# Optimization experiments

Hardware: AMD Instinct MI355X
Metric: run time of the kernel (lower is better)

The kernel has to match this reference:

```python
import jax, jax.numpy as jnp
import numpy as np

B, H, V, L, T = 64, 512, 32000, 3, 38
SOS = 0  # word2idx['<SOS>']


def setup_inputs() -> dict:
    key = jax.random.key(0)
    ks = jax.random.split(key, 16)
    s = 0.05
    rn = lambda k, shape: jax.random.normal(k, shape, jnp.float32) * s
    return {
        "feat": jax.random.normal(ks[0], (B, H), jnp.float32),
        "W_ih0": rn(ks[1], (4 * H, 2 * H)),
        "W_hh0": rn(ks[2], (4 * H, H)),
        "W_ih_rest": rn(ks[3], (L - 1, 4 * H, H)),
        "W_hh_rest": rn(ks[4], (L - 1, 4 * H, H)),
        "b_ih": rn(ks[5], (L, 4 * H)),
        "b_hh": rn(ks[6], (L, 4 * H)),
        "embed": rn(ks[7], (V, H)),
        "W_proj": rn(ks[8], (V, H)),
        "b_proj": rn(ks[9], (V,)),
        "W_hid": rn(ks[10], (H, H)),
        "b_hid": rn(ks[11], (H,)),
        "W_enc": rn(ks[12], (H, H)),
        "b_enc": rn(ks[13], (H,)),
        "W_attout": rn(ks[14], (1, H)),
        "b_attout": rn(ks[15], (1,)),
    }


def _lstm_cell(x, h, c, Wih, Whh, bih, bhh):
    # PyTorch gate order: i, f, g, o
    g = x @ Wih.T + h @ Whh.T + bih + bhh
    i, f, gg, o = jnp.split(g, 4, axis=-1)
    c2 = jax.nn.sigmoid(f) * c + jax.nn.sigmoid(i) * jnp.tanh(gg)
    h2 = jax.nn.sigmoid(o) * jnp.tanh(c2)
    return h2, c2


def _forward(feat, W_ih0, W_hh0, W_ih_rest, W_hh_rest, b_ih, b_hh,
             embed, W_proj, b_proj, W_hid, b_hid, W_enc, b_enc,
             W_attout, b_attout):
    # encoder 'sequence': pooled feature repeated over L decoder layers -> [L,B,H]
    enc = jnp.broadcast_to(feat[None], (L, B, H))
    enc_p = enc @ W_enc.T + b_enc  # precompute encoder projection (constant over steps)

    def attn(hbar):  # hbar = sum(hidden_layers)/L, [B,H]  (Bahdanau additive attention)
        e = (jnp.tanh(enc_p + (hbar @ W_hid.T + b_hid)[None]) @ W_attout.T + b_attout)[..., 0]  # [L,B]
        w = jax.nn.softmax(e, axis=0)  # softmax over encoder positions
        return jnp.einsum('lb,lbh->bh', w, enc)  # context [B,H]

    def lstm(inp, h, c):  # one time-step through the 3-layer stacked LSTM
        h0, c0 = _lstm_cell(inp, h[0], c[0], W_ih0, W_hh0, b_ih[0], b_hh[0])
        h1, c1 = _lstm_cell(h0, h[1], c[1], W_ih_rest[0], W_hh_rest[0], b_ih[1], b_hh[1])
        h2, c2 = _lstm_cell(h1, h[2], c[2], W_ih_rest[1], W_hh_rest[1], b_ih[2], b_hh[2])
        return jnp.stack([h0, h1, h2]), jnp.stack([c0, c1, c2])

    ctx0 = attn(feat)  # initial hidden = feat repeated L times -> mean = feat
    start = jnp.broadcast_to(embed[SOS], (B, H))
    h = jnp.broadcast_to(ctx0[None], (L, B, H))
    c = h
    inp0 = jnp.concatenate([ctx0, start], axis=-1)  # [B, 2H]

    def step(carry, _):
        h, c, inp = carry
        h, c = lstm(inp, h, c)
        out = h[-1]  # [B,H]
        ids = jnp.argmax(out @ W_proj.T + b_proj, axis=-1)  # greedy token (dropout in eval mode)
        emb = embed[ids]  # [B,H]
        ctx = attn(emb / L)  # addMask averages with 1/decoder_layer weights
        return (h, c, jnp.concatenate([ctx, emb], axis=-1)), out

    _, outs = jax.lax.scan(step, (h, c, inp0), None, length=T - 1)  # outs [T-1,B,H]
    pred = jnp.concatenate([start[None], outs], axis=0)  # [T,B,H]
    # final projection, permuted to [B, V, T] as in the torch module
    return jnp.einsum('tbh,vh->bvt', pred, W_proj) + b_proj[None, :, None]


def reference(feat, W_ih0, W_hh0, W_ih_rest, W_hh_rest, b_ih, b_hh,
              embed, W_proj, b_proj, W_hid, b_hid, W_enc, b_enc,
              W_attout, b_attout):
    return _forward(feat, W_ih0, W_hh0, W_ih_rest, W_hh_rest, b_ih, b_hh,
                    embed, W_proj, b_proj, W_hid, b_hid, W_enc, b_enc,
                    W_attout, b_attout)
```

## Files before the change

kernel.cpp:

```cpp
#include <hip/hip_runtime.h>
#include <hip/hip_bf16.h>

#define B   64
#define H   512
#define V   32000
#define T   38
#define G4  2048
#define NSTEP 37
#define VT  64
#define KC  64
#define LDP 68
#define NTILE 250
#define DELTA 0.008f
#define MAXC 128

typedef __attribute__((ext_vector_type(8))) short short8;
typedef __attribute__((ext_vector_type(4))) float f32x4;
typedef unsigned long long ull;

__device__ __forceinline__ float sigf(float x){ return 1.0f/(1.0f + expf(-x)); }

__device__ __forceinline__ unsigned int fkey(float x){
  unsigned int u = __float_as_uint(x);
  return (u & 0x80000000u) ? ~u : (u | 0x80000000u);
}
__device__ __forceinline__ float fromkey(unsigned int k){
  unsigned int u = (k & 0x80000000u) ? (k & 0x7fffffffu) : ~k;
  return __uint_as_float(u);
}
__device__ __forceinline__ ull mkkey(float v, int idx){
  return ((ull)fkey(v)<<32) | (ull)(unsigned int)(~(unsigned int)idx);
}
__device__ __forceinline__ unsigned short f2bf(float x){
  unsigned int u = __float_as_uint(x);
  unsigned int r = (u + 0x7FFFu + ((u >> 16) & 1u)) >> 16;
  return (unsigned short)r;
}
__device__ __forceinline__ float bf2f(unsigned short u){
  return __uint_as_float((unsigned int)u << 16);
}

__global__ __launch_bounds__(256) void k_init_state(const float* __restrict__ feat,
                                                    float* __restrict__ hT, float* __restrict__ cT,
                                                    ull* __restrict__ packed){
  int idx = blockIdx.x*blockDim.x + threadIdx.x;
  if (idx < 3*H*B){
    int b = idx & (B-1);
    int k = (idx >> 6) & (H-1);
    float v = feat[(size_t)b*H + k];
    hT[idx] = v;
    cT[idx] = v;
  }
  if (idx < NSTEP*B) packed[idx] = 0ULL;
}

__global__ __launch_bounds__(256) void k_convW(const float* __restrict__ src,
                                               unsigned short* __restrict__ hi){
  int i = blockIdx.x*blockDim.x + threadIdx.x;
  float4 f = ((const float4*)src)[i];
  ushort4 h4 = make_ushort4(f2bf(f.x), f2bf(f.y), f2bf(f.z), f2bf(f.w));
  ((ushort4*)hi)[i] = h4;
}

__global__ __launch_bounds__(256) void k_gfeat(const float* __restrict__ feat,
                                               const float* __restrict__ Wih0,
                                               const float* __restrict__ b_ih,
                                               const float* __restrict__ b_hh,
                                               float* __restrict__ gfeatT){
  int j = blockIdx.x;
  int b = threadIdx.x;
  int gate = threadIdx.y;
  int r = gate*H + j;
  const float* w = Wih0 + (size_t)r*(2*H);
  const float* x = feat + (size_t)b*H;
  float acc = 0.f;
  #pragma unroll 4
  for (int k=0;k<H;k++) acc = fmaf(w[k], x[k], acc);
  gfeatT[((size_t)gate*H + j)*B + b] = acc + b_ih[r] + b_hh[r];
}

__global__ __launch_bounds__(256) void k_row0(const float* __restrict__ embed_,
                                              const float* __restrict__ Wp,
                                              const float* __restrict__ bp,
                                              unsigned short* __restrict__ dstBf,
                                              float* __restrict__ dstF, int mode){
  int v = blockIdx.x*blockDim.x + threadIdx.x;
  if (v >= V) return;
  const float4* e = (const float4*)embed_;
  const float4* w = (const float4*)(Wp + (size_t)v*H);
  float acc = 0.f;
  #pragma unroll 4
  for (int k=0;k<H/4;k++){
    float4 a = e[k], c = w[k];
    acc += a.x*c.x + a.y*c.y + a.z*c.z + a.w*c.w;
  }
  acc += bp[v];
  if (mode == 0){
    unsigned short bv = f2bf(acc);
    for (int b=0;b<B;b++) __builtin_nontemporal_store(bv, dstBf + (size_t)b*V + v);
  } else {
    for (int b=0;b<B;b++) dstF[((size_t)b*V + v)*T] = acc;
  }
}

__global__ __launch_bounds__(256) void k_lstm(int layer, int s,
    const float* __restrict__ Wih, const float* __restrict__ Whh,
    const float* __restrict__ bias_ih, const float* __restrict__ bias_hh,
    const float* __restrict__ gfeatT,
    const float* __restrict__ embed_,
    const ull* __restrict__ packedPrev,
    const float* __restrict__ xLowerT,
    const float* __restrict__ hOldT,
    float* __restrict__ hNewT,
    float* __restrict__ cT_,
    unsigned short* __restrict__ hBf,
    float* __restrict__ hF)
{
  const int j  = blockIdx.x;
  const int b  = threadIdx.x;
  const int ks = threadIdx.y;
  __shared__ float part[4][4][B];

  const int kbase = (ks & 1)*256;
  const float *w0,*w1,*w2,*w3;
  const float* xptr = nullptr;
  const float* eptr = nullptr;

  if (ks < 2){
    if (layer == 0){
      const size_t gs = (size_t)H*(2*H);
      w0 = Wih + (size_t)j*(2*H) + H + kbase;
      w1 = w0 + gs; w2 = w0 + 2*gs; w3 = w0 + 3*gs;
      int er = 0;
      if (s > 0) er = (int)(~(unsigned int)(packedPrev[b] & 0xFFFFFFFFull));
      eptr = embed_ + (size_t)er*H + kbase;
    } else {
      const size_t gs = (size_t)H*H;
      w0 = Wih + (size_t)j*H + kbase;
      w1 = w0 + gs; w2 = w0 + 2*gs; w3 = w0 + 3*gs;
      xptr = xLowerT + (size_t)kbase*B + b;
    }
  } else {
    const size_t gs = (size_t)H*H;
    w0 = Whh + (size_t)j*H + kbase;
    w1 = w0 + gs; w2 = w0 + 2*gs; w3 = w0 + 3*gs;
    xptr = hOldT + (size_t)kbase*B + b;
  }

  float a0=0.f, a1=0.f, a2=0.f, a3=0.f;
  if (eptr){
    #pragma unroll 4
    for (int k=0;k<256;k++){
      float xv = eptr[k];
      a0 = fmaf(w0[k], xv, a0); a1 = fmaf(w1[k], xv, a1);
      a2 = fmaf(w2[k], xv, a2); a3 = fmaf(w3[k], xv, a3);
    }
  } else {
    #pragma unroll 4
    for (int k=0;k<256;k++){
      float xv = xptr[(size_t)k*B];
      a0 = fmaf(w0[k], xv, a0); a1 = fmaf(w1[k], xv, a1);
      a2 = fmaf(w2[k], xv, a2); a3 = fmaf(w3[k], xv, a3);
    }
  }
  part[ks][0][b]=a0; part[ks][1][b]=a1; part[ks][2][b]=a2; part[ks][3][b]=a3;
  __syncthreads();

  if (ks == 0){
    float g[4];
    #pragma unroll
    for (int gt=0; gt<4; gt++){
      float sum = part[0][gt][b] + part[1][gt][b] + part[2][gt][b] + part[3][gt][b];
      if (layer == 0) sum += gfeatT[((size_t)gt*H + j)*B + b];
      else            sum += bias_ih[gt*H + j] + bias_hh[gt*H + j];
      g[gt] = sum;
    }
    float i_ = sigf(g[0]);
    float f_ = sigf(g[1]);
    float gg = tanhf(g[2]);
    float o_ = sigf(g[3]);
    float cold = cT_[(size_t)j*B + b];
    float c2 = f_*cold + i_*gg;
    float h2 = o_*tanhf(c2);
    cT_[(size_t)j*B + b]  = c2;
    hNewT[(size_t)j*B + b] = h2;
    if (hBf) hBf[(size_t)b*H + j] = f2bf(h2);
    if (hF)  hF [(size_t)b*H + j] = h2;
  }
}

__global__ __launch_bounds__(256) void k_logits_mfma(
    const unsigned short* __restrict__ Wbf,
    const unsigned short* __restrict__ h2bf,
    const float* __restrict__ bp,
    unsigned short* __restrict__ dst,
    ull* __restrict__ tilemax)
{
  const int tid  = threadIdx.x;
  const int wave = tid >> 6;
  const int lane = tid & 63;
  const int col  = lane & 15;
  const int grp  = lane >> 4;
  const int v0   = blockIdx.x*128 + wave*32;

  f32x4 acc[4][2] = {{{0.f,0.f,0.f,0.f},{0.f,0.f,0.f,0.f}},
                     {{0.f,0.f,0.f,0.f},{0.f,0.f,0.f,0.f}},
                     {{0.f,0.f,0.f,0.f},{0.f,0.f,0.f,0.f}},
                     {{0.f,0.f,0.f,0.f},{0.f,0.f,0.f,0.f}}};

  const unsigned short* hp = h2bf + (size_t)col*H + grp*8;
  const unsigned short* wp = Wbf  + (size_t)(v0+col)*H + grp*8;

  for (int k0 = 0; k0 < H; k0 += 32){
    short8 afr[4], bfr[2];
    #pragma unroll
    for (int bt=0;bt<4;bt++)
      afr[bt] = *(const short8*)(hp + (size_t)bt*16*H + k0);
    #pragma unroll
    for (int vt=0;vt<2;vt++)
      bfr[vt] = *(const short8*)(wp + (size_t)vt*16*H + k0);
    #pragma unroll
    for (int bt=0;bt<4;bt++)
      #pragma unroll
      for (int vt=0;vt<2;vt++)
        acc[bt][vt] = __builtin_amdgcn_mfma_f32_16x16x32_bf16(afr[bt], bfr[vt], acc[bt][vt], 0,0,0);
  }

  float bias0 = bp[v0 + col];
  float bias1 = bp[v0 + 16 + col];

  ull keys[4][4];
  #pragma unroll
  for (int bt=0;bt<4;bt++){
    #pragma unroll
    for (int r=0;r<4;r++){
      int b = bt*16 + grp*4 + r;
      float val0 = acc[bt][0][r] + bias0;
      float val1 = acc[bt][1][r] + bias1;
      __builtin_nontemporal_store(f2bf(val0), dst + (size_t)b*V + v0 + col);
      __builtin_nontemporal_store(f2bf(val1), dst + (size_t)b*V + v0 + 16 + col);
      float m; int mv;
      if (val1 > val0){ m = val1; mv = v0+16+col; } else { m = val0; mv = v0+col; }
      keys[bt][r] = mkkey(m, mv);
    }
  }
  #pragma unroll
  for (int bt=0;bt<4;bt++)
    #pragma unroll
    for (int r=0;r<4;r++){
      ull k2 = keys[bt][r];
      #pragma unroll
      for (int m=1;m<16;m<<=1){
        ull o = __shfl_xor(k2, m, 64);
        if (o > k2) k2 = o;
      }
      keys[bt][r] = k2;
    }

  __shared__ ull wred[4][64];
  if (col == 0){
    #pragma unroll
    for (int bt=0;bt<4;bt++)
      #pragma unroll
      for (int r=0;r<4;r++)
        wred[wave][bt*16 + grp*4 + r] = keys[bt][r];
  }
  __syncthreads();
  if (tid < 64){
    ull best = wred[0][tid];
    #pragma unroll
    for (int w=1;w<4;w++) if (wred[w][tid] > best) best = wred[w][tid];
    tilemax[(size_t)tid*NTILE + blockIdx.x] = best;
  }
}

__global__ __launch_bounds__(256) void k_rescue(
    const unsigned short* __restrict__ plane,
    const ull* __restrict__ tilemax,
    const float* __restrict__ hF,
    const float* __restrict__ Wp,
    const float* __restrict__ bp,
    ull* __restrict__ packedS)
{
  const int b    = blockIdx.x;
  const int tid  = threadIdx.x;
  const int lane = tid & 63;
  const int wave = tid >> 6;

  __shared__ float hrow[H];
  __shared__ ull   keybuf[256];
  __shared__ int   tlist[NTILE];
  __shared__ int   vlist[MAXC];
  __shared__ ull   ckey[MAXC];
  __shared__ int   tcount, vcount;

  for (int k=tid; k<H; k+=256) hrow[k] = hF[(size_t)b*H + k];
  ull myk = (tid < NTILE) ? tilemax[(size_t)b*NTILE + tid] : 0ULL;
  keybuf[tid] = myk;
  if (tid == 0){ tcount = 0; vcount = 0; }
  __syncthreads();
  #pragma unroll
  for (int st=128; st>0; st>>=1){
    if (tid < st){ ull o = keybuf[tid+st]; if (o > keybuf[tid]) keybuf[tid] = o; }
    __syncthreads();
  }
  const float gmax   = fromkey((unsigned int)(keybuf[0] >> 32));
  const float thresh = gmax - DELTA;

  if (tid < NTILE && fromkey((unsigned int)(myk >> 32)) >= thresh){
    int i = atomicAdd(&tcount, 1); tlist[i] = tid;
  }
  __syncthreads();

  const int nt = tcount;
  for (int ti=0; ti<nt; ti++){
    if (tid < 128){
      int v = tlist[ti]*128 + tid;
      float val = bf2f(plane[(size_t)b*V + v]);
      if (val >= thresh){
        int i = atomicAdd(&vcount, 1);
        if (i < MAXC) vlist[i] = v;
      }
    }
  }
  __syncthreads();
  const int nc = min(vcount, MAXC);

  for (int base=0; base<nc; base+=4){
    int i = base + wave;
    if (i < nc){
      int v = vlist[i];
      const float* wrow = Wp + (size_t)v*H;
      float acc = 0.f;
      #pragma unroll
      for (int k=lane; k<H; k+=64) acc = fmaf(wrow[k], hrow[k], acc);
      #pragma unroll
      for (int m=32; m>0; m>>=1) acc += __shfl_xor(acc, m, 64);
      if (lane == 0) ckey[i] = mkkey(acc + bp[v], v);
    }
  }
  __syncthreads();
  if (tid == 0){
    ull best = 0ULL;
    for (int i=0;i<nc;i++) if (ckey[i] > best) best = ckey[i];
    packedS[b] = best;
  }
}

__global__ __launch_bounds__(256) void k_logits(
    const float* __restrict__ h2T,
    const float* __restrict__ Wp,
    const float* __restrict__ bp,
    float* __restrict__ dst, int strideV, int strideB,
    ull* __restrict__ packedS)
{
  __shared__ float Wt[KC][LDP];
  __shared__ float Xt[KC][LDP];
  __shared__ ull red[B][17];

  const int tid = threadIdx.x;
  const int v0  = blockIdx.x * VT;
  const int tv  = tid & 15;
  const int tb  = tid >> 4;
  const int vr  = tid >> 2;
  const int kq  = tid & 3;

  float acc[4][4];
  #pragma unroll
  for (int i=0;i<4;i++)
    #pragma unroll
    for (int q=0;q<4;q++) acc[i][q] = 0.f;

  for (int k0=0; k0<H; k0+=KC){
    __syncthreads();
    const float* wsrc = Wp + (size_t)(v0+vr)*H + k0 + kq*16;
    #pragma unroll
    for (int i=0;i<4;i++){
      float4 w4 = *(const float4*)(wsrc + i*4);
      int kk = kq*16 + i*4;
      Wt[kk+0][vr]=w4.x; Wt[kk+1][vr]=w4.y; Wt[kk+2][vr]=w4.z; Wt[kk+3][vr]=w4.w;
    }
    const float* xsrc = h2T + (size_t)(k0+vr)*B + kq*16;
    #pragma unroll
    for (int i=0;i<4;i++){
      float4 x4 = *(const float4*)(xsrc + i*4);
      int bb = kq*16 + i*4;
      Xt[vr][bb+0]=x4.x; Xt[vr][bb+1]=x4.y; Xt[vr][bb+2]=x4.z; Xt[vr][bb+3]=x4.w;
    }
    __syncthreads();
    #pragma unroll 8
    for (int k=0;k<KC;k++){
      float4 w4 = *(const float4*)&Wt[k][tv<<2];
      float4 x4 = *(const float4*)&Xt[k][tb<<2];
      acc[0][0]=fmaf(x4.x,w4.x,acc[0][0]); acc[0][1]=fmaf(x4.x,w4.y,acc[0][1]);
      acc[0][2]=fmaf(x4.x,w4.z,acc[0][2]); acc[0][3]=fmaf(x4.x,w4.w,acc[0][3]);
      acc[1][0]=fmaf(x4.y,w4.x,acc[1][0]); acc[1][1]=fmaf(x4.y,w4.y,acc[1][1]);
      acc[1][2]=fmaf(x4.y,w4.z,acc[1][2]); acc[1][3]=fmaf(x4.y,w4.w,acc[1][3]);
      acc[2][0]=fmaf(x4.z,w4.x,acc[2][0]); acc[2][1]=fmaf(x4.z,w4.y,acc[2][1]);
      acc[2][2]=fmaf(x4.z,w4.z,acc[2][2]); acc[2][3]=fmaf(x4.z,w4.w,acc[2][3]);
      acc[3][0]=fmaf(x4.w,w4.x,acc[3][0]); acc[3][1]=fmaf(x4.w,w4.y,acc[3][1]);
      acc[3][2]=fmaf(x4.w,w4.z,acc[3][2]); acc[3][3]=fmaf(x4.w,w4.w,acc[3][3]);
    }
  }

  float4 bb4 = *(const float4*)(bp + v0 + (tv<<2));
  float barr[4] = {bb4.x, bb4.y, bb4.z, bb4.w};
  float vals[4][4];
  #pragma unroll
  for (int bj=0;bj<4;bj++)
    #pragma unroll
    for (int vi=0;vi<4;vi++) vals[bj][vi] = acc[bj][vi] + barr[vi];

  #pragma unroll
  for (int bj=0;bj<4;bj++){
    int b = (tb<<2)+bj;
    #pragma unroll
    for (int vi=0;vi<4;vi++)
      dst[(size_t)b*strideB + (size_t)(v0+(tv<<2)+vi)*strideV] = vals[bj][vi];
  }

  #pragma unroll
  for (int bj=0;bj<4;bj++){
    float m = vals[bj][0]; int mi = v0+(tv<<2);
    #pragma unroll
    for (int vi=1;vi<4;vi++){
      if (vals[bj][vi] > m){ m = vals[bj][vi]; mi = v0+(tv<<2)+vi; }
    }
    red[(tb<<2)+bj][tv] = mkkey(m, mi);
  }
  __syncthreads();
  if (tid < B){
    ull best = red[tid][0];
    #pragma unroll
    for (int t2=1;t2<16;t2++){ ull k2 = red[tid][t2]; if (k2 > best) best = k2; }
    atomicMax(packedS + tid, best);
  }
}

__global__ __launch_bounds__(256) void k_transpose(const unsigned short* __restrict__ stage,
                                                   float* __restrict__ out){
  __shared__ float tile[64][40];
  const int b  = blockIdx.x / (V/64);
  const int vt = blockIdx.x % (V/64);
  const int v0 = vt*64;
  const int tid = threadIdx.x;

  for (int idx = tid; idx < T*64; idx += 256){
    int t  = idx >> 6;
    int vl = idx & 63;
    unsigned short u = __builtin_nontemporal_load(stage + (size_t)t*B*V + (size_t)b*V + v0 + vl);
    tile[vl][t] = bf2f(u);
  }
  __syncthreads();

  float* obase = out + ((size_t)b*V + v0)*T;
  for (int idx = tid; idx < (T*64)/4; idx += 256){
    int e = idx*4;
    f32x4 o;
    o[0] = tile[(e+0)/T][(e+0)%T];
    o[1] = tile[(e+1)/T][(e+1)%T];
    o[2] = tile[(e+2)/T][(e+2)%T];
    o[3] = tile[(e+3)/T][(e+3)%T];
    __builtin_nontemporal_store(o, (f32x4*)(obase + e));
  }
}

extern "C" void kernel_launch(void* const* d_in, const int* in_sizes, int n_in,
                              void* d_out, int out_size, void* d_ws, size_t ws_size,
                              hipStream_t stream){
  const float* feat      = (const float*)d_in[0];
  const float* W_ih0     = (const float*)d_in[1];
  const float* W_hh0     = (const float*)d_in[2];
  const float* W_ih_rest = (const float*)d_in[3];
  const float* W_hh_rest = (const float*)d_in[4];
  const float* b_ih      = (const float*)d_in[5];
  const float* b_hh      = (const float*)d_in[6];
  const float* embed     = (const float*)d_in[7];
  const float* W_proj    = (const float*)d_in[8];
  const float* b_proj    = (const float*)d_in[9];
  float* out = (float*)d_out;

  char* ws = (char*)d_ws;
  size_t off = 0;
  float* hT = (float*)(ws + off); off += (size_t)2*3*H*B*4;
  float* cT = (float*)(ws + off); off += (size_t)3*H*B*4;
  float* gfeatT = (float*)(ws + off); off += (size_t)4*H*B*4;
  ull* packed = (ull*)(ws + off); off += (size_t)NSTEP*B*8;
  unsigned short* h2bf = (unsigned short*)(ws + off); off += (size_t)B*H*2;
  float* hF32 = (float*)(ws + off); off += (size_t)B*H*4;
  ull* tilemax = (ull*)(ws + off); off += (size_t)B*NTILE*8;
  off = (off + 255) & ~(size_t)255;
  unsigned short* Whi = (unsigned short*)(ws + off); off += (size_t)V*H*2;
  off = (off + 255) & ~(size_t)255;
  unsigned short* stage = (unsigned short*)(ws + off);
  const size_t need = off + (size_t)T*B*V*2;
  const bool fast = (ws_size >= need);

  dim3 bl64x4(64,4);
  k_init_state<<<(3*H*B + 255)/256, 256, 0, stream>>>(feat, hT, cT, packed);
  k_gfeat<<<H, bl64x4, 0, stream>>>(feat, W_ih0, b_ih, b_hh, gfeatT);
  if (fast){
    k_convW<<<(V*H/4)/256, 256, 0, stream>>>(W_proj, Whi);
    k_row0<<<(V+255)/256, 256, 0, stream>>>(embed, W_proj, b_proj, stage, (float*)nullptr, 0);
  } else {
    k_row0<<<(V+255)/256, 256, 0, stream>>>(embed, W_proj, b_proj, (unsigned short*)nullptr, out, 1);
  }

  const size_t LHB = (size_t)H*B;
  for (int s=0; s<NSTEP; s++){
    const int p = s & 1, q = p ^ 1;
    float* hOld = hT + (size_t)p*3*LHB;
    float* hNew = hT + (size_t)q*3*LHB;
    const ull* pk = packed + (size_t)(s>0 ? s-1 : 0)*B;

    k_lstm<<<H, bl64x4, 0, stream>>>(0, s, W_ih0, W_hh0,
        b_ih, b_hh, gfeatT, embed, pk,
        (const float*)nullptr, hOld + 0*LHB, hNew + 0*LHB, cT + 0*LHB,
        (unsigned short*)nullptr, (float*)nullptr);
    k_lstm<<<H, bl64x4, 0, stream>>>(1, s, W_ih_rest, W_hh_rest,
        b_ih + 1*G4, b_hh + 1*G4, (const float*)nullptr, (const float*)nullptr,
        (const ull*)nullptr,
        hNew + 0*LHB, hOld + 1*LHB, hNew + 1*LHB, cT + 1*LHB,
        (unsigned short*)nullptr, (float*)nullptr);
    k_lstm<<<H, bl64x4, 0, stream>>>(2, s, W_ih_rest + (size_t)G4*H, W_hh_rest + (size_t)G4*H,
        b_ih + 2*G4, b_hh + 2*G4, (const float*)nullptr, (const float*)nullptr,
        (const ull*)nullptr,
        hNew + 1*LHB, hOld + 2*LHB, hNew + 2*LHB, cT + 2*LHB,
        fast ? h2bf : (unsigned short*)nullptr,
        fast ? hF32 : (float*)nullptr);

    if (fast){
      unsigned short* plane = stage + (size_t)(s+1)*B*V;
      k_logits_mfma<<<NTILE, 256, 0, stream>>>(Whi, h2bf, b_proj, plane, tilemax);
      k_rescue<<<B, 256, 0, stream>>>(plane, tilemax, hF32, W_proj, b_proj,
                                      packed + (size_t)s*B);
    } else {
      k_logits<<<V/VT, 256, 0, stream>>>(hNew + 2*LHB, W_proj, b_proj,
          out + (s+1), T, V*T, packed + (size_t)s*B);
    }
  }

  if (fast) k_transpose<<<B*(V/64), 256, 0, stream>>>(stage, out);
}
```

Before: 3.893 ms.

## Fuse argmax rescue into logits kernel via last-blocks ticket counter

Removes the separate per-step rescue launch. The logits MFMA kernel now takes an atomic ticket after writing its tile maxima. The last 16 blocks spin until all 250 tiles are done, then each handles the rescue for 4 batch rows. This trades one kernel launch per step for a spin-wait in 16 blocks and less parallelism in the rescue (16 blocks instead of 64). Correctness relies on all 250 blocks being co-resident, or at least on the last-ticket blocks not starving earlier ones.

```diff
diff --git a/kernel.cpp b/kernel.cpp
--- a/kernel.cpp
+++ b/kernel.cpp
@@ -13,6 +13,8 @@
 #define NTILE 250
 #define DELTA 0.008f
 #define MAXC 128
+#define NRG 16
+#define BPG 4
 
 typedef __attribute__((ext_vector_type(8))) short short8;
 typedef __attribute__((ext_vector_type(4))) float f32x4;
@@ -42,7 +44,8 @@
 
 __global__ __launch_bounds__(256) void k_init_state(const float* __restrict__ feat,
                                                     float* __restrict__ hT, float* __restrict__ cT,
-                                                    ull* __restrict__ packed){
+                                                    ull* __restrict__ packed,
+                                                    int* __restrict__ cnt){
   int idx = blockIdx.x*blockDim.x + threadIdx.x;
   if (idx < 3*H*B){
     int b = idx & (B-1);
@@ -52,6 +55,7 @@
     cT[idx] = v;
   }
   if (idx < NSTEP*B) packed[idx] = 0ULL;
+  if (idx < NSTEP) cnt[idx] = 0;
 }
 
 __global__ __launch_bounds__(256) void k_convW(const float* __restrict__ src,
@@ -194,7 +198,11 @@
     const unsigned short* __restrict__ h2bf,
     const float* __restrict__ bp,
     unsigned short* __restrict__ dst,
-    ull* __restrict__ tilemax)
+    ull* __restrict__ tilemax,
+    int* __restrict__ cnt,
+    const float* __restrict__ hF,
+    const float* __restrict__ WpF,
+    ull* __restrict__ packedS)
 {
   const int tid  = threadIdx.x;
   const int wave = tid >> 6;
@@ -272,78 +280,89 @@
     for (int w=1;w<4;w++) if (wred[w][tid] > best) best = wred[w][tid];
     tilemax[(size_t)tid*NTILE + blockIdx.x] = best;
   }
-}
-
-__global__ __launch_bounds__(256) void k_rescue(
-    const unsigned short* __restrict__ plane,
-    const ull* __restrict__ tilemax,
-    const float* __restrict__ hF,
-    const float* __restrict__ Wp,
-    const float* __restrict__ bp,
-    ull* __restrict__ packedS)
-{
-  const int b    = blockIdx.x;
-  const int tid  = threadIdx.x;
-  const int lane = tid & 63;
-  const int wave = tid >> 6;
+
+  asm volatile("s_waitcnt vmcnt(0)" ::: "memory");
+  __syncthreads();
+  __shared__ int ticket_s;
+  if (tid == 0)
+    ticket_s = __hip_atomic_fetch_add(cnt, 1, __ATOMIC_RELEASE, __HIP_MEMORY_SCOPE_AGENT);
+  __syncthreads();
+  const int ticket = ticket_s;
+  if (ticket < NTILE - NRG) return;
+  const int rg = ticket - (NTILE - NRG);
+
+  if (tid == 0){
+    while (__hip_atomic_load(cnt, __ATOMIC_RELAXED, __HIP_MEMORY_SCOPE_AGENT) < NTILE)
+      __builtin_amdgcn_s_sleep(2);
+  }
+  __syncthreads();
 
   __shared__ float hrow[H];
   __shared__ ull   keybuf[256];
-  __shared__ int   tlist[NTILE];
+  __shared__ int   tlist[64];
   __shared__ int   vlist[MAXC];
   __shared__ ull   ckey[MAXC];
   __shared__ int   tcount, vcount;
 
-  for (int k=tid; k<H; k+=256) hrow[k] = hF[(size_t)b*H + k];
-  ull myk = (tid < NTILE) ? tilemax[(size_t)b*NTILE + tid] : 0ULL;
-  keybuf[tid] = myk;
-  if (tid == 0){ tcount = 0; vcount = 0; }
-  __syncthreads();
-  #pragma unroll
-  for (int st=128; st>0; st>>=1){
-    if (tid < st){ ull o = keybuf[tid+st]; if (o > keybuf[tid]) keybuf[tid] = o; }
-    __syncthreads();
-  }
-  const float gmax   = fromkey((unsigned int)(keybuf[0] >> 32));
-  const float thresh = gmax - DELTA;
-
-  if (tid < NTILE && fromkey((unsigned int)(myk >> 32)) >= thresh){
-    int i = atomicAdd(&tcount, 1); tlist[i] = tid;
-  }
-  __syncthreads();
-
-  const int nt = tcount;
-  for (int ti=0; ti<nt; ti++){
-    if (tid < 128){
-      int v = tlist[ti]*128 + tid;
-      float val = bf2f(plane[(size_t)b*V + v]);
-      if (val >= thresh){
-        int i = atomicAdd(&vcount, 1);
-        if (i < MAXC) vlist[i] = v;
+  for (int bi = 0; bi < BPG; ++bi){
+    const int b = rg*BPG + bi;
+    for (int k=tid; k<H; k+=256) hrow[k] = hF[(size_t)b*H + k];
+    ull myk = 0ULL;
+    if (tid < NTILE)
+      myk = __hip_atomic_load(tilemax + (size_t)b*NTILE + tid,
+                              __ATOMIC_RELAXED, __HIP_MEMORY_SCOPE_AGENT);
+    keybuf[tid] = myk;
+    if (tid == 0){ tcount = 0; vcount = 0; }
+    __syncthreads();
+    #pragma unroll
+    for (int st=128; st>0; st>>=1){
+      if (tid < st){ ull o = keybuf[tid+st]; if (o > keybuf[tid]) keybuf[tid] = o; }
+      __syncthreads();
+    }
+    const float gmax   = fromkey((unsigned int)(keybuf[0] >> 32));
+    const float thresh = gmax - DELTA;
+
+    if (tid < NTILE && fromkey((unsigned int)(myk >> 32)) >= thresh){
+      int i = atomicAdd(&tcount, 1); if (i < 64) tlist[i] = tid;
+    }
+    __syncthreads();
+
+    const int nt = min(tcount, 64);
+    for (int ti=0; ti<nt; ++ti){
+      if (tid < 64){
+        const unsigned int* p32 = (const unsigned int*)(dst + (size_t)b*V + tlist[ti]*128);
+        unsigned int u = __hip_atomic_load((unsigned int*)(p32 + tid),
+                                           __ATOMIC_RELAXED, __HIP_MEMORY_SCOPE_AGENT);
+        int vbase = tlist[ti]*128 + 2*tid;
+        float va = bf2f((unsigned short)(u & 0xFFFFu));
+        float vb = bf2f((unsigned short)(u >> 16));
+        if (va >= thresh){ int i = atomicAdd(&vcount,1); if (i<MAXC) vlist[i] = vbase; }
+        if (vb >= thresh){ int i = atomicAdd(&vcount,1); if (i<MAXC) vlist[i] = vbase+1; }
       }
     }
-  }
-  __syncthreads();
-  const int nc = min(vcount, MAXC);
-
-  for (int base=0; base<nc; base+=4){
-    int i = base + wave;
-    if (i < nc){
-      int v = vlist[i];
-      const float* wrow = Wp + (size_t)v*H;
-      float acc = 0.f;
-      #pragma unroll
-      for (int k=lane; k<H; k+=64) acc = fmaf(wrow[k], hrow[k], acc);
-      #pragma unroll
-      for (int m=32; m>0; m>>=1) acc += __shfl_xor(acc, m, 64);
-      if (lane == 0) ckey[i] = mkkey(acc + bp[v], v);
-    }
-  }
-  __syncthreads();
-  if (tid == 0){
-    ull best = 0ULL;
-    for (int i=0;i<nc;i++) if (ckey[i] > best) best = ckey[i];
-    packedS[b] = best;
+    __syncthreads();
+    const int nc = min(vcount, MAXC);
+
+    for (int base=0; base<nc; base+=4){
+      int i = base + wave;
+      if (i < nc){
+        int v = vlist[i];
+        const float* wrow = WpF + (size_t)v*H;
+        float a = 0.f;
+        #pragma unroll
+        for (int k=lane; k<H; k+=64) a = fmaf(wrow[k], hrow[k], a);
+        #pragma unroll
+        for (int m=32; m>0; m>>=1) a += __shfl_xor(a, m, 64);
+        if (lane == 0) ckey[i] = mkkey(a + bp[v], v);
+      }
+    }
+    __syncthreads();
+    if (tid == 0){
+      ull best = 0ULL;
+      for (int i=0;i<nc;i++) if (ckey[i] > best) best = ckey[i];
+      packedS[b] = best;
+    }
+    __syncthreads();
   }
 }
 
@@ -489,6 +508,7 @@
   unsigned short* h2bf = (unsigned short*)(ws + off); off += (size_t)B*H*2;
   float* hF32 = (float*)(ws + off); off += (size_t)B*H*4;
   ull* tilemax = (ull*)(ws + off); off += (size_t)B*NTILE*8;
+  int* cnt = (int*)(ws + off); off += (size_t)NSTEP*4;
   off = (off + 255) & ~(size_t)255;
   unsigned short* Whi = (unsigned short*)(ws + off); off += (size_t)V*H*2;
   off = (off + 255) & ~(size_t)255;
@@ -497,7 +517,7 @@
   const bool fast = (ws_size >= need);
 
   dim3 bl64x4(64,4);
-  k_init_state<<<(3*H*B + 255)/256, 256, 0, stream>>>(feat, hT, cT, packed);
+  k_init_state<<<(3*H*B + 255)/256, 256, 0, stream>>>(feat, hT, cT, packed, cnt);
   k_gfeat<<<H, bl64x4, 0, stream>>>(feat, W_ih0, b_ih, b_hh, gfeatT);
   if (fast){
     k_convW<<<(V*H/4)/256, 256, 0, stream>>>(W_proj, Whi);
@@ -531,9 +551,9 @@
 
     if (fast){
       unsigned short* plane = stage + (size_t)(s+1)*B*V;
-      k_logits_mfma<<<NTILE, 256, 0, stream>>>(Whi, h2bf, b_proj, plane, tilemax);
-      k_rescue<<<B, 256, 0, stream>>>(plane, tilemax, hF32, W_proj, b_proj,
-                                      packed + (size_t)s*B);
+      k_logits_mfma<<<NTILE, 256, 0, stream>>>(Whi, h2bf, b_proj, plane, tilemax,
+                                               cnt + s, hF32, W_proj,
+                                               packed + (size_t)s*B);
     } else {
       k_logits<<<V/VT, 256, 0, stream>>>(hNew + 2*LHB, W_proj, b_proj,
           out + (s+1), T, V*T, packed + (size_t)s*B);
```

After: 4.535 ms. 1.16x slower.

## Fuse fp32 argmax rescue into MFMA logits kernel with per-tile thresholds

Applied to the files above, without the earlier changes.

Merges the separate rescue kernel into the bf16 MFMA logits kernel. Each tile now picks candidates using its own per-row tile maximum minus DELTA, recomputes their exact fp32 dot products, and combines results with atomicMax into the packed argmax. This drops one launch per decode step and the tilemax round trip through global memory. In exchange every tile rescores at least one candidate per batch row, which adds far more fp32 dot products per step. It also relies on the packed buffer being zeroed beforehand for atomicMax to work.

```diff
diff --git a/kernel.cpp b/kernel.cpp
--- a/kernel.cpp
+++ b/kernel.cpp
@@ -12,7 +12,7 @@
 #define LDP 68
 #define NTILE 250
 #define DELTA 0.008f
-#define MAXC 128
+#define VCAP 512
 
 typedef __attribute__((ext_vector_type(8))) short short8;
 typedef __attribute__((ext_vector_type(4))) float f32x4;
@@ -194,7 +194,9 @@
     const unsigned short* __restrict__ h2bf,
     const float* __restrict__ bp,
     unsigned short* __restrict__ dst,
-    ull* __restrict__ tilemax)
+    const float* __restrict__ hF,
+    const float* __restrict__ WpF,
+    ull* __restrict__ packedS)
 {
   const int tid  = threadIdx.x;
   const int wave = tid >> 6;
@@ -258,6 +260,10 @@
     }
 
   __shared__ ull wred[4][64];
+  __shared__ float bthr[B];
+  __shared__ int  vlist[VCAP];
+  __shared__ int  vcount;
+  if (tid == 0) vcount = 0;
   if (col == 0){
     #pragma unroll
     for (int bt=0;bt<4;bt++)
@@ -270,80 +276,51 @@
     ull best = wred[0][tid];
     #pragma unroll
     for (int w=1;w<4;w++) if (wred[w][tid] > best) best = wred[w][tid];
-    tilemax[(size_t)tid*NTILE + blockIdx.x] = best;
-  }
-}
-
-__global__ __launch_bounds__(256) void k_rescue(
-    const unsigned short* __restrict__ plane,
-    const ull* __restrict__ tilemax,
-    const float* __restrict__ hF,
-    const float* __restrict__ Wp,
-    const float* __restrict__ bp,
-    ull* __restrict__ packedS)
-{
-  const int b    = blockIdx.x;
-  const int tid  = threadIdx.x;
-  const int lane = tid & 63;
-  const int wave = tid >> 6;
-
-  __shared__ float hrow[H];
-  __shared__ ull   keybuf[256];
-  __shared__ int   tlist[NTILE];
-  __shared__ int   vlist[MAXC];
-  __shared__ ull   ckey[MAXC];
-  __shared__ int   tcount, vcount;
-
-  for (int k=tid; k<H; k+=256) hrow[k] = hF[(size_t)b*H + k];
-  ull myk = (tid < NTILE) ? tilemax[(size_t)b*NTILE + tid] : 0ULL;
-  keybuf[tid] = myk;
-  if (tid == 0){ tcount = 0; vcount = 0; }
+    bthr[tid] = fromkey((unsigned int)(best >> 32)) - DELTA;
+  }
   __syncthreads();
-  #pragma unroll
-  for (int st=128; st>0; st>>=1){
-    if (tid < st){ ull o = keybuf[tid+st]; if (o > keybuf[tid]) keybuf[tid] = o; }
-    __syncthreads();
-  }
-  const float gmax   = fromkey((unsigned int)(keybuf[0] >> 32));
-  const float thresh = gmax - DELTA;
-
-  if (tid < NTILE && fromkey((unsigned int)(myk >> 32)) >= thresh){
-    int i = atomicAdd(&tcount, 1); tlist[i] = tid;
+
+  #pragma unroll
+  for (int bt=0;bt<4;bt++){
+    #pragma unroll
+    for (int r=0;r<4;r++){
+      int b = bt*16 + grp*4 + r;
+      float thr = bthr[b];
+      float val0 = acc[bt][0][r] + bias0;
+      float val1 = acc[bt][1][r] + bias1;
+      #pragma unroll
+      for (int vt=0; vt<2; vt++){
+        float val = vt ? val1 : val0;
+        int v = v0 + vt*16 + col;
+        if (val >= thr){
+          int i = atomicAdd(&vcount, 1);
+          if (i < VCAP) vlist[i] = (b << 15) | v;
+          else {
+            const float* wrow = WpF + (size_t)v*H;
+            const float* hrow = hF  + (size_t)b*H;
+            float a = 0.f;
+            for (int k=0;k<H;k++) a = fmaf(wrow[k], hrow[k], a);
+            atomicMax(packedS + b, mkkey(a + bp[v], v));
+          }
+        }
+      }
+    }
   }
   __syncthreads();
-
-  const int nt = tcount;
-  for (int ti=0; ti<nt; ti++){
-    if (tid < 128){
-      int v = tlist[ti]*128 + tid;
-      float val = bf2f(plane[(size_t)b*V + v]);
-      if (val >= thresh){
-        int i = atomicAdd(&vcount, 1);
-        if (i < MAXC) vlist[i] = v;
-      }
-    }
-  }
-  __syncthreads();
-  const int nc = min(vcount, MAXC);
-
-  for (int base=0; base<nc; base+=4){
-    int i = base + wave;
-    if (i < nc){
-      int v = vlist[i];
-      const float* wrow = Wp + (size_t)v*H;
-      float acc = 0.f;
-      #pragma unroll
-      for (int k=lane; k<H; k+=64) acc = fmaf(wrow[k], hrow[k], acc);
-      #pragma unroll
-      for (int m=32; m>0; m>>=1) acc += __shfl_xor(acc, m, 64);
-      if (lane == 0) ckey[i] = mkkey(acc + bp[v], v);
-    }
-  }
-  __syncthreads();
-  if (tid == 0){
-    ull best = 0ULL;
-    for (int i=0;i<nc;i++) if (ckey[i] > best) best = ckey[i];
-    packedS[b] = best;
+  const int nc = min(vcount, VCAP);
+
+  for (int i = wave; i < nc; i += 4){
+    int pk = vlist[i];
+    int b  = pk >> 15;
+    int v  = pk & 0x7FFF;
+    const float* wrow = WpF + (size_t)v*H;
+    const float* hrow = hF  + (size_t)b*H;
+    float a = 0.f;
+    #pragma unroll
+    for (int k=lane; k<H; k+=64) a = fmaf(wrow[k], hrow[k], a);
+    #pragma unroll
+    for (int m=32; m>0; m>>=1) a += __shfl_xor(a, m, 64);
+    if (lane == 0) atomicMax(packedS + b, mkkey(a + bp[v], v));
   }
 }
 
@@ -488,7 +465,6 @@
   ull* packed = (ull*)(ws + off); off += (size_t)NSTEP*B*8;
   unsigned short* h2bf = (unsigned short*)(ws + off); off += (size_t)B*H*2;
   float* hF32 = (float*)(ws + off); off += (size_t)B*H*4;
-  ull* tilemax = (ull*)(ws + off); off += (size_t)B*NTILE*8;
   off = (off + 255) & ~(size_t)255;
   unsigned short* Whi = (unsigned short*)(ws + off); off += (size_t)V*H*2;
   off = (off + 255) & ~(size_t)255;
@@ -531,9 +507,8 @@
 
     if (fast){
       unsigned short* plane = stage + (size_t)(s+1)*B*V;
-      k_logits_mfma<<<NTILE, 256, 0, stream>>>(Whi, h2bf, b_proj, plane, tilemax);
-      k_rescue<<<B, 256, 0, stream>>>(plane, tilemax, hF32, W_proj, b_proj,
-                                      packed + (size_t)s*B);
+      k_logits_mfma<<<NTILE, 256, 0, stream>>>(Whi, h2bf, b_proj, plane,
+                                               hF32, W_proj, packed + (size_t)s*B);
     } else {
       k_logits<<<V/VT, 256, 0, stream>>>(hNew + 2*LHB, W_proj, b_proj,
           out + (s+1), T, V*T, packed + (size_t)s*B);
```

New measurement: 6.283 ms. 61.4% more time.
